# Optimization experiments

Hardware: AMD Instinct MI355X
Metric: run time of the kernel (lower is better)

The kernel has to match this reference:

```python
import jax, jax.numpy as jnp
import numpy as np

B, S, E, H = 4, 512, 1024, 16
DH = E // H
SCALE = 1.0 / float(np.sqrt(DH))


def setup_inputs() -> dict:
    key = jax.random.key(0)
    ks = jax.random.split(key, 6)
    x_val = jax.random.normal(ks[0], (B, S, E), dtype=jnp.float32)
    eps = 0.1 * jax.random.uniform(ks[1], (B, S, E), dtype=jnp.float32)
    x_lb = x_val - eps
    x_ub = x_val + eps
    s = 1.0 / float(np.sqrt(E))
    in_proj_w = jax.random.uniform(ks[2], (E, 3 * E), jnp.float32, -s, s)
    in_proj_b = jax.random.uniform(ks[3], (3 * E,), jnp.float32, -s, s)
    out_proj_w = jax.random.uniform(ks[4], (E, E), jnp.float32, -s, s)
    out_proj_b = jax.random.uniform(ks[5], (E,), jnp.float32, -s, s)
    return dict(x_val=x_val, x_lb=x_lb, x_ub=x_ub,
                in_proj_w=in_proj_w, in_proj_b=in_proj_b,
                out_proj_w=out_proj_w, out_proj_b=out_proj_b)


def _pos(x):
    return jnp.maximum(x, 0.0)


def _neg(x):
    return jnp.minimum(x, 0.0)


def ibp_linear(v, l, u, W, b):
    # interval input x point weight: lb' = lb@W+ + ub@W-,  ub' = ub@W+ + lb@W-
    Wp, Wn = _pos(W), _neg(W)
    return v @ W + b, l @ Wp + u @ Wn + b, u @ Wp + l @ Wn + b


def ibp_matmul(av, al, au, bv, bl, bu):
    # interval x interval matmul with the 4-way clamp decomposition (as in ibp.matmul)
    val = av @ bv
    lb = (_pos(al) @ _pos(bl) + _pos(au) @ _neg(bl)
          + _neg(al) @ _pos(bu) + _neg(au) @ _neg(bu))
    ub = (_pos(au) @ _pos(bu) + _pos(al) @ _neg(bu)
          + _neg(au) @ _pos(bl) + _neg(al) @ _neg(bl))
    return val, lb, ub


def ibp_softmax(v, l, u):
    # p_i lower bound: exp(lb_i) / (exp(lb_i) + sum_{j!=i} exp(ub_j)); symmetric for upper
    pv = jax.nn.softmax(v, axis=-1)
    m = jnp.max(u, axis=-1, keepdims=True)
    e_l = jnp.exp(l - m)
    e_u = jnp.exp(u - m)
    S_l = jnp.sum(e_l, axis=-1, keepdims=True)
    S_u = jnp.sum(e_u, axis=-1, keepdims=True)
    pl = e_l / (S_u - e_u + e_l)
    pu = e_u / (S_l - e_l + e_u)
    return pv, jnp.clip(pl, 0.0, 1.0), jnp.clip(pu, 0.0, 1.0)


def _heads(x):  # [B,S,E] -> [B,H,S,DH]
    return x.reshape(B, S, H, DH).transpose(0, 2, 1, 3)


def _merge(x):  # [B,H,S,DH] -> [B,S,E]
    return x.transpose(0, 2, 1, 3).reshape(B, S, E)


def reference(x_val, x_lb, x_ub, in_proj_w, in_proj_b, out_proj_w, out_proj_b):
    qkv_v, qkv_l, qkv_u = ibp_linear(x_val, x_lb, x_ub, in_proj_w, in_proj_b)

    def split(t):
        q, k, v = jnp.split(t, 3, axis=-1)
        return _heads(q), _heads(k), _heads(v)

    (qv, kv, vv) = split(qkv_v)
    (ql, kl, vl) = split(qkv_l)
    (qu, ku, vu) = split(qkv_u)
    # positive scalar scale preserves bound ordering
    qv, ql, qu = qv * SCALE, ql * SCALE, qu * SCALE
    kT = lambda x: x.transpose(0, 1, 3, 2)
    sv, sl, su = ibp_matmul(qv, ql, qu, kT(kv), kT(kl), kT(ku))  # [B,H,S,S]
    pv, pl, pu = ibp_softmax(sv, sl, su)
    ov, ol, ou = ibp_matmul(pv, pl, pu, vv, vl, vu)  # [B,H,S,DH]
    ov, ol, ou = _merge(ov), _merge(ol), _merge(ou)
    yv, yl, yu = ibp_linear(ov, ol, ou, out_proj_w, out_proj_b)
    return jnp.stack([yv, yl, yu])  # [3,B,S,E]
```

## Files before the change

kernel.cpp:

```cpp
#include <hip/hip_runtime.h>
#include <math.h>

#define SEQ    512
#define EMB    1024
#define NHEAD  16
#define DHEAD  64
#define NBAT   4
#define QSCALE 0.125f
#define KS     72
#define VS     40

typedef __attribute__((ext_vector_type(8))) short bf16x8;
typedef __attribute__((ext_vector_type(4))) float f32x4;

#define MFMA16(a, b, c) __builtin_amdgcn_mfma_f32_16x16x32_bf16(a, b, c, 0, 0, 0)

__device__ __forceinline__ unsigned short f2b(float x) {
  union { float f; unsigned int u; } a; a.f = x;
  unsigned int u = a.u;
  unsigned int r = (u + 0x7fffu + ((u >> 16) & 1u)) >> 16;
  return (unsigned short)r;
}
__device__ __forceinline__ unsigned short f2b_fast(float x) {
  union { float f; unsigned int u; } a; a.f = x;
  return (unsigned short)((a.u + 0x8000u) >> 16);
}
__device__ __forceinline__ float b2f(unsigned short x) {
  union { unsigned int u; float f; } a; a.u = ((unsigned int)x) << 16; return a.f;
}

__device__ __forceinline__ void async16(const unsigned short* g, unsigned short* lds) {
  __builtin_amdgcn_global_load_lds(
      (const __attribute__((address_space(1))) unsigned int*)g,
      (__attribute__((address_space(3))) unsigned int*)lds, 16, 0, 0);
}

__device__ __forceinline__ void clamp_pn8(bf16x8 x, bf16x8* p, bf16x8* n) {
  const unsigned int* xu = (const unsigned int*)&x;
  unsigned int* pp = (unsigned int*)p;
  unsigned int* nn = (unsigned int*)n;
#pragma unroll
  for (int e = 0; e < 4; e++) {
    const unsigned int s = xu[e] & 0x80008000u;
    const unsigned int mask = s | (s - (s >> 15));
    nn[e] = xu[e] & mask;
    pp[e] = xu[e] & ~mask;
  }
}

__device__ __forceinline__ float wave16_sum(float x) {
#pragma unroll
  for (int m = 1; m <= 8; m <<= 1) x += __shfl_xor(x, m);
  return x;
}

__global__ __launch_bounds__(256)
void convert_stack(const float* __restrict__ v, const float* __restrict__ l,
                   const float* __restrict__ u,
                   unsigned short* __restrict__ outV,
                   unsigned short* __restrict__ outC,
                   unsigned short* __restrict__ outR, int total4)
{
  int i = blockIdx.x * 256 + threadIdx.x;
  if (i >= total4) return;
  float4 v4 = ((const float4*)v)[i];
  float4 l4 = ((const float4*)l)[i];
  float4 u4 = ((const float4*)u)[i];
  float lv[4] = {l4.x, l4.y, l4.z, l4.w};
  float uv[4] = {u4.x, u4.y, u4.z, u4.w};
  float vv[4] = {v4.x, v4.y, v4.z, v4.w};
  ushort4 ov, oc, orr;
  unsigned short* pv = (unsigned short*)&ov;
  unsigned short* pc = (unsigned short*)&oc;
  unsigned short* pr = (unsigned short*)&orr;
#pragma unroll
  for (int e = 0; e < 4; e++) {
    pv[e] = f2b(vv[e]);
    pc[e] = f2b(0.5f * (lv[e] + uv[e]));
    pr[e] = f2b(0.5f * (uv[e] - lv[e]));
  }
  ((ushort4*)outV)[i] = ov;
  ((ushort4*)outC)[i] = oc;
  ((ushort4*)outR)[i] = orr;
}

__global__ __launch_bounds__(256)
void wt_convert(const float* __restrict__ W,
                unsigned short* __restrict__ Wt,
                unsigned short* __restrict__ Wa, int K, int N)
{
  __shared__ float tile[32][33];
  const int n0 = blockIdx.x * 32, k0 = blockIdx.y * 32;
  const int tx = threadIdx.x, ty = threadIdx.y;
#pragma unroll
  for (int r = 0; r < 32; r += 8)
    tile[ty + r][tx] = W[(size_t)(k0 + ty + r) * N + n0 + tx];
  __syncthreads();
#pragma unroll
  for (int r = 0; r < 32; r += 8) {
    const float w = tile[tx][ty + r];
    const size_t o = (size_t)(n0 + ty + r) * K + k0 + tx;
    Wt[o] = f2b(w);
    Wa[o] = f2b(fabsf(w));
  }
}

template<int BN>
__global__ __launch_bounds__(256, 2)
void gemm_ibp3(const unsigned short* __restrict__ Av,
               const unsigned short* __restrict__ Ac,
               const unsigned short* __restrict__ Ar,
               const unsigned short* __restrict__ Bt,
               const unsigned short* __restrict__ Ba,
               int K, const float* __restrict__ bias,
               float* __restrict__ oV, float* __restrict__ oL, float* __restrict__ oU,
               unsigned short* __restrict__ hV, unsigned short* __restrict__ hL,
               unsigned short* __restrict__ hU,
               unsigned short* __restrict__ vtV, unsigned short* __restrict__ vtL,
               unsigned short* __restrict__ vtU, int N)
{
  constexpr int NF = BN / 32;
  __shared__ __attribute__((aligned(16))) unsigned short Avs[2][64 * 32];
  __shared__ __attribute__((aligned(16))) unsigned short Acs[2][64 * 32];
  __shared__ __attribute__((aligned(16))) unsigned short Ars[2][64 * 32];
  __shared__ __attribute__((aligned(16))) unsigned short Bts[2][BN * 32];
  __shared__ __attribute__((aligned(16))) unsigned short Bas[2][BN * 32];

  const int t = threadIdx.x, lane = t & 63, w = t >> 6;
  const int m0 = blockIdx.y * 64, n0 = blockIdx.x * BN;
  const int wm = w & 1, wn = w >> 1;
  const int quad = lane >> 4, r16 = lane & 15;
  const int srow = lane >> 2, sseg = lane & 3;

  f32x4 av[2][NF], ac[2][NF], ar[2][NF];
#pragma unroll
  for (int i = 0; i < 2; i++)
#pragma unroll
    for (int j = 0; j < NF; j++) {
      av[i][j] = (f32x4){0.f, 0.f, 0.f, 0.f};
      ac[i][j] = (f32x4){0.f, 0.f, 0.f, 0.f};
      ar[i][j] = (f32x4){0.f, 0.f, 0.f, 0.f};
    }

  const int iters = K >> 5;
  auto stage = [&](int it, int buf) {
    const int k0 = it * 32;
    const size_t ga = (size_t)(m0 + 16 * w + srow) * K + k0 + sseg * 8;
    async16(Av + ga, &Avs[buf][16 * w * 32]);
    async16(Ac + ga, &Acs[buf][16 * w * 32]);
    async16(Ar + ga, &Ars[buf][16 * w * 32]);
#pragma unroll
    for (int r = 0; r < BN / 64; r++) {
      const int brow = (BN / 4) * w + 16 * r;
      const size_t gb = (size_t)(n0 + brow + srow) * K + k0 + sseg * 8;
      async16(Bt + gb, &Bts[buf][brow * 32]);
      async16(Ba + gb, &Bas[buf][brow * 32]);
    }
  };

  stage(0, 0);
  for (int it = 0; it < iters; ++it) {
    const int cur = it & 1;
    __syncthreads();
    if (it + 1 < iters) stage(it + 1, cur ^ 1);
    bf16x8 fv[2], fc[2], fr[2], gt[NF], gb[NF];
#pragma unroll
    for (int i = 0; i < 2; i++) {
      const int off = (wm * 32 + i * 16 + r16) * 32 + quad * 8;
      fv[i] = *(const bf16x8*)(&Avs[cur][off]);
      fc[i] = *(const bf16x8*)(&Acs[cur][off]);
      fr[i] = *(const bf16x8*)(&Ars[cur][off]);
    }
#pragma unroll
    for (int j = 0; j < NF; j++) {
      const int off = (wn * (BN / 2) + j * 16 + r16) * 32 + quad * 8;
      gt[j] = *(const bf16x8*)(&Bts[cur][off]);
      gb[j] = *(const bf16x8*)(&Bas[cur][off]);
    }
#pragma unroll
    for (int i = 0; i < 2; i++)
#pragma unroll
      for (int j = 0; j < NF; j++) {
        av[i][j] = MFMA16(fv[i], gt[j], av[i][j]);
        ac[i][j] = MFMA16(fc[i], gt[j], ac[i][j]);
        ar[i][j] = MFMA16(fr[i], gb[j], ar[i][j]);
      }
  }

#pragma unroll
  for (int i = 0; i < 2; i++) {
    const int mbase = m0 + wm * 32 + i * 16 + quad * 4;
#pragma unroll
    for (int j = 0; j < NF; j++) {
      const int n = n0 + wn * (BN / 2) + j * 16 + r16;
      const float bv = bias[n];
      float vv[4], lv[4], uv[4];
#pragma unroll
      for (int rI = 0; rI < 4; rI++) {
        const float c = ac[i][j][rI], r = ar[i][j][rI];
        vv[rI] = av[i][j][rI] + bv;
        lv[rI] = c - r + bv;
        uv[rI] = c + r + bv;
      }
      if (hV) {
#pragma unroll
        for (int rI = 0; rI < 4; rI++) {
          hV[(size_t)(mbase + rI) * N + n] = f2b(vv[rI]);
          hL[(size_t)(mbase + rI) * N + n] = f2b(lv[rI]);
          hU[(size_t)(mbase + rI) * N + n] = f2b(uv[rI]);
        }
      } else {
#pragma unroll
        for (int rI = 0; rI < 4; rI++) {
          oV[(size_t)(mbase + rI) * N + n] = vv[rI];
          oL[(size_t)(mbase + rI) * N + n] = lv[rI];
          oU[(size_t)(mbase + rI) * N + n] = uv[rI];
        }
      }
      if (vtV && n >= 2048) {
        const int hh = (n - 2048) >> 6, dd = (n - 2048) & 63;
        const int bb = mbase >> 9, ss = mbase & 511;
        ushort4 v4, l4, u4;
        unsigned short* vp = (unsigned short*)&v4;
        unsigned short* lp = (unsigned short*)&l4;
        unsigned short* up = (unsigned short*)&u4;
#pragma unroll
        for (int rI = 0; rI < 4; rI++) {
          vp[rI] = f2b(vv[rI]); lp[rI] = f2b(lv[rI]); up[rI] = f2b(uv[rI]);
        }
        const size_t vo = (size_t)((bb * 16 + hh) * 64 + dd) * 512 + ss;
        *(ushort4*)(vtV + vo) = v4;
        *(ushort4*)(vtL + vo) = l4;
        *(ushort4*)(vtU + vo) = u4;
      }
    }
  }
}

__device__ __forceinline__ void qk_tile(const unsigned short* K0,
                                        const unsigned short* K1,
                                        const unsigned short* K2,
                                        int cl, int quad,
                                        const bf16x8 qvf[2], const bf16x8 qlpf[2],
                                        const bf16x8 qlnf[2], const bf16x8 qupf[2],
                                        const bf16x8 qunf[2],
                                        f32x4* avp, f32x4* alp, f32x4* aup)
{
  f32x4 v = {0.f, 0.f, 0.f, 0.f}, l = v, u = v;
#pragma unroll
  for (int kh = 0; kh < 2; kh++) {
    const int off = cl * KS + kh * 32 + quad * 8;
    bf16x8 kv = *(const bf16x8*)(K0 + off);
    bf16x8 kl = *(const bf16x8*)(K1 + off);
    bf16x8 ku = *(const bf16x8*)(K2 + off);
    bf16x8 klp, kln, kup, kun;
    clamp_pn8(kl, &klp, &kln);
    clamp_pn8(ku, &kup, &kun);
    v = MFMA16(qvf[kh], kv, v);
    l = MFMA16(qlpf[kh], klp, l);
    l = MFMA16(qupf[kh], kln, l);
    l = MFMA16(qlnf[kh], kup, l);
    l = MFMA16(qunf[kh], kun, l);
    u = MFMA16(qupf[kh], kup, u);
    u = MFMA16(qlpf[kh], kun, u);
    u = MFMA16(qunf[kh], klp, u);
    u = MFMA16(qlnf[kh], kln, u);
  }
  *avp = v; *alp = l; *aup = u;
}

__global__ __launch_bounds__(256, 4)
void ibp_attn_qk(const unsigned short* __restrict__ qkv_v,
                 const unsigned short* __restrict__ qkv_l,
                 const unsigned short* __restrict__ qkv_u,
                 uint2* __restrict__ eVb, uint2* __restrict__ eLb,
                 uint2* __restrict__ eUb, float4* __restrict__ sums)
{
  __shared__ __attribute__((aligned(16))) unsigned short Kd[2][3 * 2304];
  __shared__ float st[2][32][3];

  const int qblk = blockIdx.x, h = blockIdx.y, b = blockIdx.z;
  const int t = threadIdx.x, lane = t & 63, w = t >> 6;
  const int wm = w >> 1, wc = w & 1;
  const int quad = lane >> 4, r16 = lane & 15;
  const int mq = b * SEQ + qblk * 32;
  const int bh = b * NHEAD + h;

  bf16x8 qvf[2], qlpf[2], qlnf[2], qupf[2], qunf[2];
  {
    const size_t qrow = (size_t)(mq + wm * 16 + r16) * 3072 + h * 64;
#pragma unroll
    for (int kh = 0; kh < 2; kh++) {
      bf16x8 v8 = *(const bf16x8*)(qkv_v + qrow + kh * 32 + quad * 8);
      bf16x8 l8 = *(const bf16x8*)(qkv_l + qrow + kh * 32 + quad * 8);
      bf16x8 u8 = *(const bf16x8*)(qkv_u + qrow + kh * 32 + quad * 8);
      const unsigned short* vs = (const unsigned short*)&v8;
      const unsigned short* ls = (const unsigned short*)&l8;
      const unsigned short* us = (const unsigned short*)&u8;
      unsigned short* ov = (unsigned short*)&qvf[kh];
      unsigned short* lp = (unsigned short*)&qlpf[kh];
      unsigned short* ln = (unsigned short*)&qlnf[kh];
      unsigned short* up = (unsigned short*)&qupf[kh];
      unsigned short* un = (unsigned short*)&qunf[kh];
#pragma unroll
      for (int e = 0; e < 8; e++) {
        ov[e] = f2b(b2f(vs[e]) * QSCALE);
        const float lf = b2f(ls[e]) * QSCALE;
        const float uf = b2f(us[e]) * QSCALE;
        lp[e] = f2b(fmaxf(lf, 0.f)); ln[e] = f2b(fminf(lf, 0.f));
        up[e] = f2b(fmaxf(uf, 0.f)); un[e] = f2b(fminf(uf, 0.f));
      }
    }
  }

  const int cl = wc * 16 + r16;
  const int krow = t >> 3, kseg = t & 7;

  float Svp[4] = {0.f, 0.f, 0.f, 0.f};
  float Slp[4] = {0.f, 0.f, 0.f, 0.f};
  float Sup[4] = {0.f, 0.f, 0.f, 0.f};

  uint4 kN0, kN1, kN2;
  {
    const size_t gk = (size_t)(b * SEQ + krow) * 3072 + 1024 + h * 64 + kseg * 8;
    kN0 = *(const uint4*)(qkv_v + gk);
    kN1 = *(const uint4*)(qkv_l + gk);
    kN2 = *(const uint4*)(qkv_u + gk);
    unsigned short* d = &Kd[0][krow * KS + kseg * 8];
    *(uint4*)d = kN0;
    *(uint4*)(d + 2304) = kN1;
    *(uint4*)(d + 4608) = kN2;
  }
  __syncthreads();

  const size_t ebase = (size_t)((bh * 16 + qblk) * 16) * 256 + t;

  for (int ct = 0; ct < 16; ct++) {
    const int cur = ct & 1;
    if (ct < 15) {
      const size_t gk = (size_t)(b * SEQ + (ct + 1) * 32 + krow) * 3072 + 1024
                        + h * 64 + kseg * 8;
      kN0 = *(const uint4*)(qkv_v + gk);
      kN1 = *(const uint4*)(qkv_l + gk);
      kN2 = *(const uint4*)(qkv_u + gk);
    }
    f32x4 av, al, au;
    qk_tile(&Kd[cur][0], &Kd[cur][2304], &Kd[cur][4608], cl, quad,
            qvf, qlpf, qlnf, qupf, qunf, &av, &al, &au);
    float ev[4], el[4], eu[4];
#pragma unroll
    for (int r = 0; r < 4; r++) {
      ev[r] = __expf(av[r]); Svp[r] += ev[r];
      el[r] = __expf(al[r]); Slp[r] += el[r];
      eu[r] = __expf(au[r]); Sup[r] += eu[r];
    }
    const size_t eo = ebase + (size_t)ct * 256;
    uint2 d;
    d.x = (unsigned int)f2b(ev[0]) | ((unsigned int)f2b(ev[1]) << 16);
    d.y = (unsigned int)f2b(ev[2]) | ((unsigned int)f2b(ev[3]) << 16);
    eVb[eo] = d;
    d.x = (unsigned int)f2b(el[0]) | ((unsigned int)f2b(el[1]) << 16);
    d.y = (unsigned int)f2b(el[2]) | ((unsigned int)f2b(el[3]) << 16);
    eLb[eo] = d;
    d.x = (unsigned int)f2b(eu[0]) | ((unsigned int)f2b(eu[1]) << 16);
    d.y = (unsigned int)f2b(eu[2]) | ((unsigned int)f2b(eu[3]) << 16);
    eUb[eo] = d;
    if (ct < 15) {
      unsigned short* dd = &Kd[cur ^ 1][krow * KS + kseg * 8];
      *(uint4*)dd = kN0;
      *(uint4*)(dd + 2304) = kN1;
      *(uint4*)(dd + 4608) = kN2;
      __syncthreads();
    }
  }

#pragma unroll
  for (int r = 0; r < 4; r++) {
    Svp[r] = wave16_sum(Svp[r]);
    Slp[r] = wave16_sum(Slp[r]);
    Sup[r] = wave16_sum(Sup[r]);
  }
  if (r16 == 0) {
#pragma unroll
    for (int r = 0; r < 4; r++) {
      st[wc][wm * 16 + quad * 4 + r][0] = Svp[r];
      st[wc][wm * 16 + quad * 4 + r][1] = Slp[r];
      st[wc][wm * 16 + quad * 4 + r][2] = Sup[r];
    }
  }
  __syncthreads();
  if (t < 32) {
    float4 s;
    s.x = st[0][t][0] + st[1][t][0];
    s.y = st[0][t][1] + st[1][t][1];
    s.z = st[0][t][2] + st[1][t][2];
    s.w = 0.f;
    sums[(size_t)bh * 512 + qblk * 32 + t] = s;
  }
}

__global__ __launch_bounds__(256, 4)
void ibp_attn_pv(const uint2* __restrict__ eVb, const uint2* __restrict__ eLb,
                 const uint2* __restrict__ eUb, const float4* __restrict__ sums,
                 const unsigned short* __restrict__ vt_v,
                 const unsigned short* __restrict__ vt_l,
                 const unsigned short* __restrict__ vt_u,
                 unsigned short* __restrict__ Ov,
                 unsigned short* __restrict__ Oc,
                 unsigned short* __restrict__ Or)
{
  __shared__ __attribute__((aligned(16))) unsigned short Vd[2][3 * 2560];
  __shared__ __attribute__((aligned(16))) unsigned short Ps[3 * 1280];

  const int qblk = blockIdx.x, h = blockIdx.y, b = blockIdx.z;
  const int t = threadIdx.x, lane = t & 63, w = t >> 6;
  const int wm = w >> 1, wc = w & 1;
  const int quad = lane >> 4, r16 = lane & 15;
  const int mq = b * SEQ + qblk * 32;
  const int bh = b * NHEAD + h;
  const int cl = wc * 16 + r16;
  const int vrow = t >> 2, vseg = t & 3;

  float rSv4[4], Sl4[4], Su4[4];
#pragma unroll
  for (int r = 0; r < 4; r++) {
    const float4 s = sums[(size_t)bh * 512 + qblk * 32 + wm * 16 + quad * 4 + r];
    rSv4[r] = 1.f / s.x;
    Sl4[r] = s.y;
    Su4[r] = s.z;
  }

  const size_t ebase = (size_t)((bh * 16 + qblk) * 16) * 256 + t;
  const size_t gvbase = (size_t)(bh * 64 + vrow) * 512 + vseg * 8;

  uint4 vN0 = *(const uint4*)(vt_v + gvbase);
  uint4 vN1 = *(const uint4*)(vt_l + gvbase);
  uint4 vN2 = *(const uint4*)(vt_u + gvbase);
  uint2 eC0 = eVb[ebase], eC1 = eLb[ebase], eC2 = eUb[ebase];
  {
    unsigned short* d = &Vd[0][vrow * VS + vseg * 8];
    *(uint4*)d = vN0;
    *(uint4*)(d + 2560) = vN1;
    *(uint4*)(d + 5120) = vN2;
  }
  __syncthreads();

  f32x4 oa[3][2];
#pragma unroll
  for (int bo = 0; bo < 3; bo++)
#pragma unroll
    for (int ds = 0; ds < 2; ds++) oa[bo][ds] = (f32x4){0.f, 0.f, 0.f, 0.f};

  for (int ct = 0; ct < 16; ct++) {
    const int cur = ct & 1;
    uint2 eN0, eN1, eN2;
    if (ct < 15) {
      const size_t gv = gvbase + (ct + 1) * 32;
      vN0 = *(const uint4*)(vt_v + gv);
      vN1 = *(const uint4*)(vt_l + gv);
      vN2 = *(const uint4*)(vt_u + gv);
      const size_t eo = ebase + (size_t)(ct + 1) * 256;
      eN0 = eVb[eo]; eN1 = eLb[eo]; eN2 = eUb[eo];
    }

    const unsigned int nvx = __shfl_xor(eC0.x, 1);
    const unsigned int nvy = __shfl_xor(eC0.y, 1);
    const float el0 = b2f((unsigned short)(eC1.x & 0xFFFFu));
    const float el1 = b2f((unsigned short)(eC1.x >> 16));
    const float el2 = b2f((unsigned short)(eC1.y & 0xFFFFu));
    const float el3 = b2f((unsigned short)(eC1.y >> 16));
    const float eu0 = b2f((unsigned short)(eC2.x & 0xFFFFu));
    const float eu1 = b2f((unsigned short)(eC2.x >> 16));
    const float eu2 = b2f((unsigned short)(eC2.y & 0xFFFFu));
    const float eu3 = b2f((unsigned short)(eC2.y >> 16));
    float pl[4], pu[4];
    pl[0] = el0 * __builtin_amdgcn_rcpf(Su4[0] - eu0 + el0);
    pu[0] = eu0 * __builtin_amdgcn_rcpf(Sl4[0] - el0 + eu0);
    pl[1] = el1 * __builtin_amdgcn_rcpf(Su4[1] - eu1 + el1);
    pu[1] = eu1 * __builtin_amdgcn_rcpf(Sl4[1] - el1 + eu1);
    pl[2] = el2 * __builtin_amdgcn_rcpf(Su4[2] - eu2 + el2);
    pu[2] = eu2 * __builtin_amdgcn_rcpf(Sl4[2] - el2 + eu2);
    pl[3] = el3 * __builtin_amdgcn_rcpf(Su4[3] - eu3 + el3);
    pu[3] = eu3 * __builtin_amdgcn_rcpf(Sl4[3] - el3 + eu3);
#pragma unroll
    for (int r = 0; r < 4; r++) {
      pl[r] = fminf(fmaxf(pl[r], 0.f), 1.f);
      pu[r] = fminf(fmaxf(pu[r], 0.f), 1.f);
    }
    const unsigned int dl0 = (unsigned int)f2b_fast(pl[0]) | ((unsigned int)f2b_fast(pl[1]) << 16);
    const unsigned int dl1 = (unsigned int)f2b_fast(pl[2]) | ((unsigned int)f2b_fast(pl[3]) << 16);
    const unsigned int du0 = (unsigned int)f2b_fast(pu[0]) | ((unsigned int)f2b_fast(pu[1]) << 16);
    const unsigned int du1 = (unsigned int)f2b_fast(pu[2]) | ((unsigned int)f2b_fast(pu[3]) << 16);
    const unsigned int nl0 = __shfl_xor(dl0, 1), nl1 = __shfl_xor(dl1, 1);
    const unsigned int nu0 = __shfl_xor(du0, 1), nu1 = __shfl_xor(du1, 1);
    if (!(r16 & 1)) {
      const int rb = (wm * 16 + quad * 4) * VS + cl;
      *(unsigned int*)(Ps + rb)               = (eC0.x & 0xFFFFu) | (nvx << 16);
      *(unsigned int*)(Ps + rb + VS)          = (eC0.x >> 16) | (nvx & 0xFFFF0000u);
      *(unsigned int*)(Ps + rb + 2 * VS)      = (eC0.y & 0xFFFFu) | (nvy << 16);
      *(unsigned int*)(Ps + rb + 3 * VS)      = (eC0.y >> 16) | (nvy & 0xFFFF0000u);
      *(unsigned int*)(Ps + 1280 + rb)          = (dl0 & 0xFFFFu) | (nl0 << 16);
      *(unsigned int*)(Ps + 1280 + rb + VS)     = (dl0 >> 16) | (nl0 & 0xFFFF0000u);
      *(unsigned int*)(Ps + 1280 + rb + 2 * VS) = (dl1 & 0xFFFFu) | (nl1 << 16);
      *(unsigned int*)(Ps + 1280 + rb + 3 * VS) = (dl1 >> 16) | (nl1 & 0xFFFF0000u);
      *(unsigned int*)(Ps + 2560 + rb)          = (du0 & 0xFFFFu) | (nu0 << 16);
      *(unsigned int*)(Ps + 2560 + rb + VS)     = (du0 >> 16) | (nu0 & 0xFFFF0000u);
      *(unsigned int*)(Ps + 2560 + rb + 2 * VS) = (du1 & 0xFFFFu) | (nu1 << 16);
      *(unsigned int*)(Ps + 2560 + rb + 3 * VS) = (du1 >> 16) | (nu1 & 0xFFFF0000u);
    }
    __syncthreads();

#pragma unroll
    for (int ds = 0; ds < 2; ds++) {
      const int dsub = wc * 2 + ds;
      const int voff = (dsub * 16 + r16) * VS + quad * 8;
      bf16x8 vv = *(const bf16x8*)(&Vd[cur][voff]);
      bf16x8 vl = *(const bf16x8*)(&Vd[cur][2560 + voff]);
      bf16x8 vu = *(const bf16x8*)(&Vd[cur][5120 + voff]);
      bf16x8 vlp, vln, vup, vun;
      clamp_pn8(vl, &vlp, &vln);
      clamp_pn8(vu, &vup, &vun);
      const int arow = (wm * 16 + r16) * VS + quad * 8;
      bf16x8 pav = *(const bf16x8*)(Ps + arow);
      bf16x8 pal = *(const bf16x8*)(Ps + 1280 + arow);
      bf16x8 pau = *(const bf16x8*)(Ps + 2560 + arow);
      oa[0][ds] = MFMA16(pav, vv, oa[0][ds]);
      oa[1][ds] = MFMA16(pal, vlp, oa[1][ds]);
      oa[1][ds] = MFMA16(pau, vln, oa[1][ds]);
      oa[2][ds] = MFMA16(pau, vup, oa[2][ds]);
      oa[2][ds] = MFMA16(pal, vun, oa[2][ds]);
    }

    if (ct < 15) {
      unsigned short* d = &Vd[cur ^ 1][vrow * VS + vseg * 8];
      *(uint4*)d = vN0;
      *(uint4*)(d + 2560) = vN1;
      *(uint4*)(d + 5120) = vN2;
      eC0 = eN0; eC1 = eN1; eC2 = eN2;
    }
    __syncthreads();
  }

#pragma unroll
  for (int ds = 0; ds < 2; ds++) {
    const int dsub = wc * 2 + ds;
#pragma unroll
    for (int r = 0; r < 4; r++) {
      const size_t row = (size_t)(mq + wm * 16 + quad * 4 + r);
      const int col = h * 64 + dsub * 16 + r16;
      const float ovv = oa[0][ds][r] * rSv4[r];
      const float olv = oa[1][ds][r];
      const float ouv = oa[2][ds][r];
      Ov[row * 1024 + col] = f2b(ovv);
      Oc[row * 1024 + col] = f2b(0.5f * (olv + ouv));
      Or[row * 1024 + col] = f2b(0.5f * (ouv - olv));
    }
  }
}

__global__ __launch_bounds__(256, 4)
void ibp_attn_mfma(const unsigned short* __restrict__ qkv_v,
                   const unsigned short* __restrict__ qkv_l,
                   const unsigned short* __restrict__ qkv_u,
                   const unsigned short* __restrict__ vt_v,
                   const unsigned short* __restrict__ vt_l,
                   const unsigned short* __restrict__ vt_u,
                   unsigned short* __restrict__ Ov,
                   unsigned short* __restrict__ Oc,
                   unsigned short* __restrict__ Or)
{
  __shared__ __attribute__((aligned(16))) unsigned short pool[6912 + 7680 + 3840];
  __shared__ float st[2][32][3];
  unsigned short* Ks = pool;
  unsigned short* Vs = pool + 6912;
  unsigned short* Psl = pool + 6912 + 7680;

  const int qblk = blockIdx.x, h = blockIdx.y, b = blockIdx.z;
  const int t = threadIdx.x, lane = t & 63, w = t >> 6;
  const int wm = w >> 1, wc = w & 1;
  const int quad = lane >> 4, r16 = lane & 15;
  const int mq = b * SEQ + qblk * 32;
  const int bh = b * NHEAD + h;

  bf16x8 qvf[2], qlpf[2], qlnf[2], qupf[2], qunf[2];
  {
    const size_t qrow = (size_t)(mq + wm * 16 + r16) * 3072 + h * 64;
#pragma unroll
    for (int kh = 0; kh < 2; kh++) {
      bf16x8 v8 = *(const bf16x8*)(qkv_v + qrow + kh * 32 + quad * 8);
      bf16x8 l8 = *(const bf16x8*)(qkv_l + qrow + kh * 32 + quad * 8);
      bf16x8 u8 = *(const bf16x8*)(qkv_u + qrow + kh * 32 + quad * 8);
      const unsigned short* vs = (const unsigned short*)&v8;
      const unsigned short* ls = (const unsigned short*)&l8;
      const unsigned short* us = (const unsigned short*)&u8;
      unsigned short* ov = (unsigned short*)&qvf[kh];
      unsigned short* lp = (unsigned short*)&qlpf[kh];
      unsigned short* ln = (unsigned short*)&qlnf[kh];
      unsigned short* up = (unsigned short*)&qupf[kh];
      unsigned short* un = (unsigned short*)&qunf[kh];
#pragma unroll
      for (int e = 0; e < 8; e++) {
        ov[e] = f2b(b2f(vs[e]) * QSCALE);
        const float lf = b2f(ls[e]) * QSCALE;
        const float uf = b2f(us[e]) * QSCALE;
        lp[e] = f2b(fmaxf(lf, 0.f)); ln[e] = f2b(fminf(lf, 0.f));
        up[e] = f2b(fmaxf(uf, 0.f)); un[e] = f2b(fminf(uf, 0.f));
      }
    }
  }

  const int cl = wc * 16 + r16;
  const int krow = t >> 3, kseg = t & 7;
  const int vrow = t >> 2, vseg = t & 3;
  const unsigned short* kplane[3] = {qkv_v, qkv_l, qkv_u};
  const unsigned short* vplane[3] = {vt_v, vt_l, vt_u};

  float Svp[4] = {0.f, 0.f, 0.f, 0.f};
  float Slp[4] = {0.f, 0.f, 0.f, 0.f};
  float Sup[4] = {0.f, 0.f, 0.f, 0.f};

#pragma unroll
  for (int pI = 0; pI < 3; pI++)
    *(uint4*)(Ks + pI * 2304 + krow * KS + kseg * 8) =
        *(const uint4*)(kplane[pI] + (size_t)(b * SEQ + krow) * 3072 + 1024 + h * 64 + kseg * 8);
  __syncthreads();

  for (int ct = 0; ct < 16; ct++) {
    const unsigned short* cur = (ct & 1) ? Vs : Ks;
    if (ct < 15) {
      unsigned short* nxt = (ct & 1) ? Ks : Vs;
      const int c0n = (ct + 1) * 32;
#pragma unroll
      for (int pI = 0; pI < 3; pI++)
        *(uint4*)(nxt + pI * 2304 + krow * KS + kseg * 8) =
            *(const uint4*)(kplane[pI] + (size_t)(b * SEQ + c0n + krow) * 3072 + 1024 + h * 64 + kseg * 8);
    }
    f32x4 av, al, au;
    qk_tile(cur, cur + 2304, cur + 4608, cl, quad,
            qvf, qlpf, qlnf, qupf, qunf, &av, &al, &au);
#pragma unroll
    for (int r = 0; r < 4; r++) {
      Svp[r] += __expf(av[r]);
      Slp[r] += __expf(al[r]);
      Sup[r] += __expf(au[r]);
    }
    __syncthreads();
  }

#pragma unroll
  for (int r = 0; r < 4; r++) {
    Svp[r] = wave16_sum(Svp[r]);
    Slp[r] = wave16_sum(Slp[r]);
    Sup[r] = wave16_sum(Sup[r]);
  }
  if (r16 == 0) {
#pragma unroll
    for (int r = 0; r < 4; r++) {
      st[wc][wm * 16 + quad * 4 + r][0] = Svp[r];
      st[wc][wm * 16 + quad * 4 + r][1] = Slp[r];
      st[wc][wm * 16 + quad * 4 + r][2] = Sup[r];
    }
  }
  __syncthreads();
  float rSv4[4], Sl4[4], Su4[4];
#pragma unroll
  for (int r = 0; r < 4; r++) {
    const int row = wm * 16 + quad * 4 + r;
    rSv4[r] = 1.f / (st[0][row][0] + st[1][row][0]);
    Sl4[r]  = st[0][row][1] + st[1][row][1];
    Su4[r]  = st[0][row][2] + st[1][row][2];
  }

  f32x4 oa[3][2];
#pragma unroll
  for (int bo = 0; bo < 3; bo++)
#pragma unroll
    for (int ds = 0; ds < 2; ds++) oa[bo][ds] = (f32x4){0.f, 0.f, 0.f, 0.f};

  for (int ct = 0; ct < 16; ct++) {
    const int c0 = ct * 32;
    __syncthreads();
#pragma unroll
    for (int pI = 0; pI < 3; pI++) {
      *(uint4*)(Ks + pI * 2304 + krow * KS + kseg * 8) =
          *(const uint4*)(kplane[pI] + (size_t)(b * SEQ + c0 + krow) * 3072 + 1024 + h * 64 + kseg * 8);
      *(uint4*)(Vs + pI * 2560 + vrow * VS + vseg * 8) =
          *(const uint4*)(vplane[pI] + (size_t)(bh * 64 + vrow) * 512 + c0 + vseg * 8);
    }
    __syncthreads();

    f32x4 av, al, au;
    qk_tile(Ks, Ks + 2304, Ks + 4608, cl, quad,
            qvf, qlpf, qlnf, qupf, qunf, &av, &al, &au);
#pragma unroll
    for (int r = 0; r < 4; r++) {
      const float ev = __expf(av[r]);
      const float el = __expf(al[r]);
      const float eu = __expf(au[r]);
      float pl = el * __builtin_amdgcn_rcpf(Su4[r] - eu + el);
      float pu = eu * __builtin_amdgcn_rcpf(Sl4[r] - el + eu);
      pl = fminf(fmaxf(pl, 0.f), 1.f);
      pu = fminf(fmaxf(pu, 0.f), 1.f);
      const float pev = __shfl_xor(ev, 1);
      const float ppl = __shfl_xor(pl, 1);
      const float ppu = __shfl_xor(pu, 1);
      if (!(r16 & 1)) {
        const unsigned int wv = (unsigned int)f2b_fast(ev) | ((unsigned int)f2b_fast(pev) << 16);
        const unsigned int wl = (unsigned int)f2b_fast(pl) | ((unsigned int)f2b_fast(ppl) << 16);
        const unsigned int wu = (unsigned int)f2b_fast(pu) | ((unsigned int)f2b_fast(ppu) << 16);
        const int prow = (wm * 16 + quad * 4 + r) * VS + cl;
        *(unsigned int*)(Psl + prow)        = wv;
        *(unsigned int*)(Psl + 1280 + prow) = wl;
        *(unsigned int*)(Psl + 2560 + prow) = wu;
      }
    }
    __syncthreads();

#pragma unroll
    for (int ds = 0; ds < 2; ds++) {
      const int dsub = wc * 2 + ds;
      const int voff = (dsub * 16 + r16) * VS + quad * 8;
      bf16x8 vv = *(const bf16x8*)(Vs + voff);
      bf16x8 vl = *(const bf16x8*)(Vs + 2560 + voff);
      bf16x8 vu = *(const bf16x8*)(Vs + 5120 + voff);
      bf16x8 vlp, vln, vup, vun;
      clamp_pn8(vl, &vlp, &vln);
      clamp_pn8(vu, &vup, &vun);
      const int arow = (wm * 16 + r16) * VS + quad * 8;
      bf16x8 pav = *(const bf16x8*)(Psl + arow);
      bf16x8 pal = *(const bf16x8*)(Psl + 1280 + arow);
      bf16x8 pau = *(const bf16x8*)(Psl + 2560 + arow);
      oa[0][ds] = MFMA16(pav, vv, oa[0][ds]);
      oa[1][ds] = MFMA16(pal, vlp, oa[1][ds]);
      oa[1][ds] = MFMA16(pau, vln, oa[1][ds]);
      oa[2][ds] = MFMA16(pau, vup, oa[2][ds]);
      oa[2][ds] = MFMA16(pal, vun, oa[2][ds]);
    }
  }

#pragma unroll
  for (int ds = 0; ds < 2; ds++) {
    const int dsub = wc * 2 + ds;
#pragma unroll
    for (int r = 0; r < 4; r++) {
      const size_t row = (size_t)(mq + wm * 16 + quad * 4 + r);
      const int col = h * 64 + dsub * 16 + r16;
      const float ovv = oa[0][ds][r] * rSv4[r];
      const float olv = oa[1][ds][r];
      const float ouv = oa[2][ds][r];
      Ov[row * 1024 + col] = f2b(ovv);
      Oc[row * 1024 + col] = f2b(0.5f * (olv + ouv));
      Or[row * 1024 + col] = f2b(0.5f * (ouv - olv));
    }
  }
}

extern "C" void kernel_launch(void* const* d_in, const int* in_sizes, int n_in,
                              void* d_out, int out_size, void* d_ws, size_t ws_size,
                              hipStream_t stream)
{
  const float* x_val = (const float*)d_in[0];
  const float* x_lb  = (const float*)d_in[1];
  const float* x_ub  = (const float*)d_in[2];
  const float* Wi    = (const float*)d_in[3];
  const float* bi    = (const float*)d_in[4];
  const float* Wo    = (const float*)d_in[5];
  const float* bo    = (const float*)d_in[6];
  float* out = (float*)d_out;

  char* p = (char*)d_ws;
  unsigned short* Xv  = (unsigned short*)p; p += (size_t)2048 * 1024 * 2;
  unsigned short* Xc  = (unsigned short*)p; p += (size_t)2048 * 1024 * 2;
  unsigned short* Xr  = (unsigned short*)p; p += (size_t)2048 * 1024 * 2;
  unsigned short* Wit = (unsigned short*)p; p += (size_t)3072 * 1024 * 2;
  unsigned short* Wia = (unsigned short*)p; p += (size_t)3072 * 1024 * 2;
  unsigned short* Wot = (unsigned short*)p; p += (size_t)1024 * 1024 * 2;
  unsigned short* Woa = (unsigned short*)p; p += (size_t)1024 * 1024 * 2;
  unsigned short* qv  = (unsigned short*)p; p += (size_t)2048 * 3072 * 2;
  unsigned short* ql  = (unsigned short*)p; p += (size_t)2048 * 3072 * 2;
  unsigned short* qu  = (unsigned short*)p; p += (size_t)2048 * 3072 * 2;
  unsigned short* Vtv = (unsigned short*)p; p += (size_t)64 * 64 * 512 * 2;
  unsigned short* Vtl = (unsigned short*)p; p += (size_t)64 * 64 * 512 * 2;
  unsigned short* Vtu = (unsigned short*)p; p += (size_t)64 * 64 * 512 * 2;
  uint2* eVb = (uint2*)p;  p += (size_t)1024 * 16 * 256 * 8;
  uint2* eLb = (uint2*)p;  p += (size_t)1024 * 16 * 256 * 8;
  uint2* eUb = (uint2*)p;  p += (size_t)1024 * 16 * 256 * 8;
  float4* sums = (float4*)p; p += (size_t)64 * 512 * 16;
  const size_t need = (size_t)(p - (char*)d_ws);

  convert_stack<<<2048, 256, 0, stream>>>(x_val, x_lb, x_ub, Xv, Xc, Xr, 524288);
  wt_convert<<<dim3(96, 32), dim3(32, 8), 0, stream>>>(Wi, Wit, Wia, 1024, 3072);
  wt_convert<<<dim3(32, 32), dim3(32, 8), 0, stream>>>(Wo, Wot, Woa, 1024, 1024);

  gemm_ibp3<128><<<dim3(3072 / 128, 32), 256, 0, stream>>>(
      Xv, Xc, Xr, Wit, Wia, 1024, bi,
      nullptr, nullptr, nullptr, qv, ql, qu, Vtv, Vtl, Vtu, 3072);

  if (ws_size >= need) {
    ibp_attn_qk<<<dim3(SEQ / 32, NHEAD, NBAT), 256, 0, stream>>>(
        qv, ql, qu, eVb, eLb, eUb, sums);
    ibp_attn_pv<<<dim3(SEQ / 32, NHEAD, NBAT), 256, 0, stream>>>(
        eVb, eLb, eUb, sums, Vtv, Vtl, Vtu, Xv, Xc, Xr);
  } else {
    ibp_attn_mfma<<<dim3(SEQ / 32, NHEAD, NBAT), 256, 0, stream>>>(
        qv, ql, qu, Vtv, Vtl, Vtu, Xv, Xc, Xr);
  }

  gemm_ibp3<64><<<dim3(1024 / 64, 32), 256, 0, stream>>>(
      Xv, Xc, Xr, Wot, Woa, 1024, bo,
      out, out + (size_t)2048 * 1024, out + (size_t)4096 * 1024,
      nullptr, nullptr, nullptr, nullptr, nullptr, nullptr, 1024);
}
```

Measured before the change: 288.4 us.

## Triple-buffer IBP GEMM with square tiles and explicit waitcnt pipelining

Rewrites the interval GEMM as a templated kernel with square BM×BN tiles. The QKV projection now uses 128×128 tiles with 8 waves instead of 64×128 with 4. LDS staging goes from double to triple buffering, prefetching two stages ahead, and uses explicit s_waitcnt vmcnt plus s_barrier in place of __syncthreads. The aim is to hide global-load latency and raise operand reuse per block. The cost is more LDS per block (up to 144KB for 128 tiles), which may lower occupancy, and a hand-tuned vmcnt count that has to match the number of loads issued per stage.

```diff
diff --git a/kernel.cpp b/kernel.cpp
--- a/kernel.cpp
+++ b/kernel.cpp
@@ -105,38 +105,41 @@
   }
 }
 
-template<int BN>
-__global__ __launch_bounds__(256, 2)
-void gemm_ibp3(const unsigned short* __restrict__ Av,
-               const unsigned short* __restrict__ Ac,
-               const unsigned short* __restrict__ Ar,
-               const unsigned short* __restrict__ Bt,
-               const unsigned short* __restrict__ Ba,
-               int K, const float* __restrict__ bias,
-               float* __restrict__ oV, float* __restrict__ oL, float* __restrict__ oU,
-               unsigned short* __restrict__ hV, unsigned short* __restrict__ hL,
-               unsigned short* __restrict__ hU,
-               unsigned short* __restrict__ vtV, unsigned short* __restrict__ vtL,
-               unsigned short* __restrict__ vtU, int N)
+template<int BM, int NW>
+__global__ __launch_bounds__(NW * 64, 2)
+void gemm_ibp3t(const unsigned short* __restrict__ Av,
+                const unsigned short* __restrict__ Ac,
+                const unsigned short* __restrict__ Ar,
+                const unsigned short* __restrict__ Bt,
+                const unsigned short* __restrict__ Ba,
+                int K, const float* __restrict__ bias,
+                float* __restrict__ oV, float* __restrict__ oL, float* __restrict__ oU,
+                unsigned short* __restrict__ hV, unsigned short* __restrict__ hL,
+                unsigned short* __restrict__ hU,
+                unsigned short* __restrict__ vtV, unsigned short* __restrict__ vtL,
+                unsigned short* __restrict__ vtU, int N)
 {
-  constexpr int NF = BN / 32;
-  __shared__ __attribute__((aligned(16))) unsigned short Avs[2][64 * 32];
-  __shared__ __attribute__((aligned(16))) unsigned short Acs[2][64 * 32];
-  __shared__ __attribute__((aligned(16))) unsigned short Ars[2][64 * 32];
-  __shared__ __attribute__((aligned(16))) unsigned short Bts[2][BN * 32];
-  __shared__ __attribute__((aligned(16))) unsigned short Bas[2][BN * 32];
+  constexpr int BN = BM;
+  constexpr int WN = NW / 2;
+  constexpr int MI = BM / 32;
+  constexpr int NJ = BN / (WN * 16);
+  __shared__ __attribute__((aligned(16))) unsigned short Avs[3][BM * 32];
+  __shared__ __attribute__((aligned(16))) unsigned short Acs[3][BM * 32];
+  __shared__ __attribute__((aligned(16))) unsigned short Ars[3][BM * 32];
+  __shared__ __attribute__((aligned(16))) unsigned short Bts[3][BN * 32];
+  __shared__ __attribute__((aligned(16))) unsigned short Bas[3][BN * 32];
 
   const int t = threadIdx.x, lane = t & 63, w = t >> 6;
-  const int m0 = blockIdx.y * 64, n0 = blockIdx.x * BN;
+  const int m0 = blockIdx.y * BM, n0 = blockIdx.x * BN;
   const int wm = w & 1, wn = w >> 1;
   const int quad = lane >> 4, r16 = lane & 15;
-  const int srow = lane >> 2, sseg = lane & 3;
-
-  f32x4 av[2][NF], ac[2][NF], ar[2][NF];
-#pragma unroll
-  for (int i = 0; i < 2; i++)
-#pragma unroll
-    for (int j = 0; j < NF; j++) {
+  const int srow = t >> 2, sseg = t & 3;
+
+  f32x4 av[MI][NJ], ac[MI][NJ], ar[MI][NJ];
+#pragma unroll
+  for (int i = 0; i < MI; i++)
+#pragma unroll
+    for (int j = 0; j < NJ; j++) {
       av[i][j] = (f32x4){0.f, 0.f, 0.f, 0.f};
       ac[i][j] = (f32x4){0.f, 0.f, 0.f, 0.f};
       ar[i][j] = (f32x4){0.f, 0.f, 0.f, 0.f};
@@ -145,54 +148,64 @@
   const int iters = K >> 5;
   auto stage = [&](int it, int buf) {
     const int k0 = it * 32;
-    const size_t ga = (size_t)(m0 + 16 * w + srow) * K + k0 + sseg * 8;
-    async16(Av + ga, &Avs[buf][16 * w * 32]);
-    async16(Ac + ga, &Acs[buf][16 * w * 32]);
-    async16(Ar + ga, &Ars[buf][16 * w * 32]);
-#pragma unroll
-    for (int r = 0; r < BN / 64; r++) {
-      const int brow = (BN / 4) * w + 16 * r;
-      const size_t gb = (size_t)(n0 + brow + srow) * K + k0 + sseg * 8;
-      async16(Bt + gb, &Bts[buf][brow * 32]);
-      async16(Ba + gb, &Bas[buf][brow * 32]);
-    }
+    const size_t ga = (size_t)(m0 + srow) * K + k0 + sseg * 8;
+    async16(Av + ga, &Avs[buf][w * 16 * 32]);
+    async16(Ac + ga, &Acs[buf][w * 16 * 32]);
+    async16(Ar + ga, &Ars[buf][w * 16 * 32]);
+    const size_t gb = (size_t)(n0 + srow) * K + k0 + sseg * 8;
+    async16(Bt + gb, &Bts[buf][w * 16 * 32]);
+    async16(Ba + gb, &Bas[buf][w * 16 * 32]);
   };
 
-  stage(0, 0);
-  for (int it = 0; it < iters; ++it) {
-    const int cur = it & 1;
-    __syncthreads();
-    if (it + 1 < iters) stage(it + 1, cur ^ 1);
-    bf16x8 fv[2], fc[2], fr[2], gt[NF], gb[NF];
-#pragma unroll
-    for (int i = 0; i < 2; i++) {
-      const int off = (wm * 32 + i * 16 + r16) * 32 + quad * 8;
+  auto body = [&](int cur) {
+    bf16x8 fv[MI], fc[MI], fr[MI], gt[NJ], gbb[NJ];
+#pragma unroll
+    for (int i = 0; i < MI; i++) {
+      const int off = (wm * (MI * 16) + i * 16 + r16) * 32 + quad * 8;
       fv[i] = *(const bf16x8*)(&Avs[cur][off]);
       fc[i] = *(const bf16x8*)(&Acs[cur][off]);
       fr[i] = *(const bf16x8*)(&Ars[cur][off]);
     }
 #pragma unroll
-    for (int j = 0; j < NF; j++) {
-      const int off = (wn * (BN / 2) + j * 16 + r16) * 32 + quad * 8;
-      gt[j] = *(const bf16x8*)(&Bts[cur][off]);
-      gb[j] = *(const bf16x8*)(&Bas[cur][off]);
-    }
-#pragma unroll
-    for (int i = 0; i < 2; i++)
-#pragma unroll
-      for (int j = 0; j < NF; j++) {
-        av[i][j] = MFMA16(fv[i], gt[j], av[i][j]);
-        ac[i][j] = MFMA16(fc[i], gt[j], ac[i][j]);
-        ar[i][j] = MFMA16(fr[i], gb[j], ar[i][j]);
+    for (int j = 0; j < NJ; j++) {
+      const int off = (wn * (NJ * 16) + j * 16 + r16) * 32 + quad * 8;
+      gt[j]  = *(const bf16x8*)(&Bts[cur][off]);
+      gbb[j] = *(const bf16x8*)(&Bas[cur][off]);
+    }
+#pragma unroll
+    for (int i = 0; i < MI; i++)
+#pragma unroll
+      for (int j = 0; j < NJ; j++) {
+        av[i][j] = MFMA16(fv[i], gt[j],  av[i][j]);
+        ac[i][j] = MFMA16(fc[i], gt[j],  ac[i][j]);
+        ar[i][j] = MFMA16(fr[i], gbb[j], ar[i][j]);
       }
-  }
-
-#pragma unroll
-  for (int i = 0; i < 2; i++) {
-    const int mbase = m0 + wm * 32 + i * 16 + quad * 4;
-#pragma unroll
-    for (int j = 0; j < NF; j++) {
-      const int n = n0 + wn * (BN / 2) + j * 16 + r16;
+  };
+
+  stage(0, 0);
+  stage(1, 1);
+  int cur = 0;
+  for (int it = 0; it < iters; ++it) {
+    __builtin_amdgcn_sched_barrier(0);
+    if (it + 1 < iters)
+      asm volatile("s_waitcnt vmcnt(5) lgkmcnt(0)" ::: "memory");
+    else
+      asm volatile("s_waitcnt vmcnt(0) lgkmcnt(0)" ::: "memory");
+    __builtin_amdgcn_s_barrier();
+    if (it + 2 < iters) {
+      int nb = cur + 2; if (nb >= 3) nb -= 3;
+      stage(it + 2, nb);
+    }
+    body(cur);
+    cur = (cur == 2) ? 0 : cur + 1;
+  }
+
+#pragma unroll
+  for (int i = 0; i < MI; i++) {
+    const int mbase = m0 + wm * (MI * 16) + i * 16 + quad * 4;
+#pragma unroll
+    for (int j = 0; j < NJ; j++) {
+      const int n = n0 + wn * (NJ * 16) + j * 16 + r16;
       const float bv = bias[n];
       float vv[4], lv[4], uv[4];
 #pragma unroll
@@ -792,7 +805,7 @@
   wt_convert<<<dim3(96, 32), dim3(32, 8), 0, stream>>>(Wi, Wit, Wia, 1024, 3072);
   wt_convert<<<dim3(32, 32), dim3(32, 8), 0, stream>>>(Wo, Wot, Woa, 1024, 1024);
 
-  gemm_ibp3<128><<<dim3(3072 / 128, 32), 256, 0, stream>>>(
+  gemm_ibp3t<128, 8><<<dim3(3072 / 128, 2048 / 128), 512, 0, stream>>>(
       Xv, Xc, Xr, Wit, Wia, 1024, bi,
       nullptr, nullptr, nullptr, qv, ql, qu, Vtv, Vtl, Vtu, 3072);
 
@@ -806,7 +819,7 @@
         qv, ql, qu, Vtv, Vtl, Vtu, Xv, Xc, Xr);
   }
 
-  gemm_ibp3<64><<<dim3(1024 / 64, 32), 256, 0, stream>>>(
+  gemm_ibp3t<64, 4><<<dim3(1024 / 64, 2048 / 64), 256, 0, stream>>>(
       Xv, Xc, Xr, Wot, Woa, 1024, bo,
       out, out + (size_t)2048 * 1024, out + (size_t)4096 * 1024,
       nullptr, nullptr, nullptr, nullptr, nullptr, nullptr, 1024);
```

New measurement: 303.5 us. 5.2% more time.
